# Kernel optimization log

Hardware: AMD Instinct MI355X
Metric: run time of the kernel (lower is better)

## Reference

```python
import jax, jax.numpy as jnp
import numpy as np

B, T, E = 4, 2048, 1024
H, D = 16, 64  # num_heads, head_size; H*D == E


def setup_inputs() -> dict:
    key = jax.random.key(0)
    ks = jax.random.split(key, 8)
    s = 0.02
    x = jax.random.normal(ks[0], (B, T, E), dtype=jnp.float32)
    attention_mask = jnp.ones((B, T), dtype=jnp.float32)
    # stacked per-head projection weights (no bias), torch Linear: y = x @ W.T
    Wq = jax.random.normal(ks[1], (H, E, D), dtype=jnp.float32) * s
    Wk = jax.random.normal(ks[2], (H, E, D), dtype=jnp.float32) * s
    Wv = jax.random.normal(ks[3], (H, E, D), dtype=jnp.float32) * s
    Wo = jax.random.normal(ks[4], (E, E), dtype=jnp.float32) * s
    bo = jnp.zeros((E,), dtype=jnp.float32)
    return {"x": x, "attention_mask": attention_mask, "Wq": Wq, "Wk": Wk,
            "Wv": Wv, "Wo": Wo, "bo": bo}


def reference(x, attention_mask, Wq, Wk, Wv, Wo, bo):
    # per-head projections, vectorized over heads: [B,T,E] x [H,E,D] -> [B,H,T,D]
    q = jnp.einsum('bte,hed->bhtd', x, Wq)
    k = jnp.einsum('bte,hed->bhtd', x, Wk)
    v = jnp.einsum('bte,hed->bhtd', x, Wv)
    scores = jnp.einsum('bhtd,bhsd->bhts', q, k) / jnp.sqrt(jnp.float32(D))
    # causal mask (tril): masked_fill with -inf
    causal = jnp.tril(jnp.ones((T, T), dtype=bool))
    scores = jnp.where(causal[None, None, :, :], scores, -jnp.inf)
    # padding mask: weights += (1 - mask) * finfo(float32).min, broadcast over queries
    neg = jnp.finfo(jnp.float32).min
    scores = scores + ((1.0 - attention_mask) * neg)[:, None, None, :]
    weights = jax.nn.softmax(scores, axis=-1)
    out = jnp.einsum('bhts,bhsd->bthd', weights, v).reshape(B, T, H * D)
    return out @ Wo.T + bo
```

## Files before the change

### kernel.cpp

```cpp
#include <hip/hip_runtime.h>
#include <hip/hip_bf16.h>

#define B_ 4
#define T_ 2048
#define E_ 1024
#define H_ 16
#define D_ 64
#define M_ (B_*T_)

typedef short bf16x8 __attribute__((ext_vector_type(8)));
typedef float f32x4  __attribute__((ext_vector_type(4)));
typedef float f32x16 __attribute__((ext_vector_type(16)));

__device__ __forceinline__ short f2bf(float f) {
    __hip_bfloat16 h = __float2bfloat16(f);
    return *reinterpret_cast<short*>(&h);
}

__device__ __forceinline__ void async_ld16(const void* g, void* l) {
    __builtin_amdgcn_global_load_lds(
        (const __attribute__((address_space(1))) unsigned int*)g,
        (__attribute__((address_space(3))) unsigned int*)l, 16, 0, 0);
}

__global__ void conv_bf16(const float* __restrict__ src, short* __restrict__ dst) {
    const int i = blockIdx.x * 256 + threadIdx.x;
    float4 v = ((const float4*)src)[i];
    short4 o = make_short4(f2bf(v.x), f2bf(v.y), f2bf(v.z), f2bf(v.w));
    ((short4*)dst)[i] = o;
}

__global__ void bias_prep(const float* __restrict__ mask, float* __restrict__ bias) {
    const int i = blockIdx.x * 256 + threadIdx.x;
    float bm = (1.0f - mask[i]) * -3.402823466e38f;
    bias[i] = fmaf(bm, 1.4426950f, -8.6561700f);
}

__global__ void wtrans(const float* __restrict__ Wq,
                       const float* __restrict__ Wk,
                       const float* __restrict__ Wv,
                       short* __restrict__ Wt) {
    const int which = blockIdx.z;
    const float* __restrict__ W = (which == 0) ? Wq : (which == 1) ? Wk : Wv;
    const int h  = blockIdx.y;
    const int e0 = blockIdx.x * 64;

    __shared__ float tile[64][65];
    const int tid = threadIdx.x;

#pragma unroll
    for (int r = 0; r < 4; ++r) {
        int lin = tid + r * 256;
        int er = lin >> 4, c4 = (lin & 15) * 4;
        float4 v = *(const float4*)(W + ((size_t)h * E_ + e0 + er) * D_ + c4);
        tile[er][c4 + 0] = v.x; tile[er][c4 + 1] = v.y;
        tile[er][c4 + 2] = v.z; tile[er][c4 + 3] = v.w;
    }
    __syncthreads();
#pragma unroll
    for (int r = 0; r < 4; ++r) {
        int lin = tid + r * 256;
        int dr = lin >> 4, j4 = (lin & 15) * 4;
        short4 o = make_short4(f2bf(tile[j4 + 0][dr]), f2bf(tile[j4 + 1][dr]),
                               f2bf(tile[j4 + 2][dr]), f2bf(tile[j4 + 3][dr]));
        *(short4*)(Wt + ((size_t)which * 1024 + h * 64 + dr) * E_ + e0 + j4) = o;
    }
}

template <int MODE>
__global__ __launch_bounds__(512, 2) void mfma_gemm(
        const short* __restrict__ A,
        const short* __restrict__ Bt,
        short* __restrict__ qo, short* __restrict__ ko, short* __restrict__ vo,
        float* __restrict__ Cout, const float* __restrict__ bo) {
    __shared__ __align__(16) char lds[3 * 49152];

    const int tid  = threadIdx.x;
    const int wave = tid >> 6, lane = tid & 63;
    const int c = lane & 15, quad = lane >> 4;
    const int wm = wave >> 1, wn = wave & 1;
    const int m0 = blockIdx.x * 256;
    const int n0 = blockIdx.y * 128;

    const int rr = tid >> 3;
    const int cc = (tid & 7) ^ (rr & 7);

    int aoff[4], boff[4];
#pragma unroll
    for (int mi = 0; mi < 4; ++mi) {
        int row = wm * 64 + mi * 16 + c;
        aoff[mi] = row * 128 + ((quad ^ (row & 7)) << 4);
    }
#pragma unroll
    for (int ni = 0; ni < 4; ++ni) {
        int row = wn * 64 + ni * 16 + c;
        boff[ni] = 32768 + row * 128 + ((quad ^ (row & 7)) << 4);
    }

    f32x4 acc[4][4] = {};

#define STGU(bufb, k0v, u) do {                                              \
        const short* _s = ((u) < 4) ? A : Bt;                                \
        const int _b0 = ((u) < 4) ? (m0 + (u) * 64) : (n0 + ((u) - 4) * 64); \
        const int _do = ((u) < 4) ? ((u) * 8192) : (32768 + ((u) - 4) * 8192);\
        async_ld16(_s + (size_t)(_b0 + rr) * 1024 + (k0v) + cc * 8,          \
                   lds + (bufb) + _do + wave * 1024);                        \
    } while (0)

#pragma unroll
    for (int u = 0; u < 6; ++u) STGU(0, 0, u);
#pragma unroll
    for (int u = 0; u < 6; ++u) STGU(49152, 64, u);
    asm volatile("s_waitcnt vmcnt(6)" ::: "memory");
    __builtin_amdgcn_s_barrier();

    int rbase = 0;
#pragma unroll 1
    for (int k = 0; k < 16; ++k) {
        const char* rb = lds + rbase;
        const int wbase = (rbase == 0) ? 98304 : rbase - 49152;
        const int kw = (k + 2) * 64;

        if (k < 14) {
            STGU(wbase, kw, 0); STGU(wbase, kw, 1);
            STGU(wbase, kw, 2); STGU(wbase, kw, 3);
            STGU(wbase, kw, 4); STGU(wbase, kw, 5);
        }

        bf16x8 a_[4][2], b_[4][2];
#pragma unroll
        for (int mi = 0; mi < 4; ++mi)
#pragma unroll
            for (int ks = 0; ks < 2; ++ks)
                a_[mi][ks] = *(const bf16x8*)(rb + (aoff[mi] ^ (ks << 6)));
#pragma unroll
        for (int ni = 0; ni < 4; ++ni)
#pragma unroll
            for (int ks = 0; ks < 2; ++ks)
                b_[ni][ks] = *(const bf16x8*)(rb + (boff[ni] ^ (ks << 6)));

        __builtin_amdgcn_s_setprio(1);
#pragma unroll
        for (int mi = 0; mi < 4; ++mi)
#pragma unroll
            for (int ni = 0; ni < 4; ++ni)
#pragma unroll
                for (int ks = 0; ks < 2; ++ks)
                    acc[mi][ni] = __builtin_amdgcn_mfma_f32_16x16x32_bf16(
                        a_[mi][ks], b_[ni][ks], acc[mi][ni], 0, 0, 0);
        __builtin_amdgcn_s_setprio(0);

        if (k < 14)       asm volatile("s_waitcnt vmcnt(6)" ::: "memory");
        else if (k == 14) asm volatile("s_waitcnt vmcnt(0)" ::: "memory");
        if (k < 15) __builtin_amdgcn_s_barrier();

        rbase = (rbase == 98304) ? 0 : rbase + 49152;
    }
#undef STGU

    if (MODE == 0) {
        const int which = n0 >> 10;
        const int nb = n0 & 1023;
        if (which == 2) {
#pragma unroll
            for (int mi = 0; mi < 4; ++mi) {
                const int m = m0 + wm * 64 + mi * 16 + quad * 4;
                const int b = m >> 11, t = m & 2047;
#pragma unroll
                for (int ni = 0; ni < 4; ++ni) {
                    const int n = nb + wn * 64 + ni * 16 + c;
                    const int h = n >> 6, d = n & 63;
                    short4 s4 = make_short4(f2bf(acc[mi][ni][0]), f2bf(acc[mi][ni][1]),
                                            f2bf(acc[mi][ni][2]), f2bf(acc[mi][ni][3]));
                    *(short4*)(vo + (((size_t)b * H_ + h) * D_ + d) * T_ + t) = s4;
                }
            }
        } else {
            short* __restrict__ outp = (which == 0) ? qo : ko;
            const float sc = (which == 0) ? 0.18033688f : 1.0f;
#pragma unroll
            for (int mi = 0; mi < 4; ++mi) {
#pragma unroll
                for (int i = 0; i < 4; ++i) {
                    const int m = m0 + wm * 64 + mi * 16 + quad * 4 + i;
                    const int b = m >> 11, t = m & 2047;
#pragma unroll
                    for (int ni = 0; ni < 4; ++ni) {
                        const int n = nb + wn * 64 + ni * 16 + c;
                        const int h = n >> 6, d = n & 63;
                        outp[(((size_t)b * H_ + h) * T_ + t) * D_ + d] =
                            f2bf(acc[mi][ni][i] * sc);
                    }
                }
            }
        }
    } else {
#pragma unroll
        for (int mi = 0; mi < 4; ++mi) {
#pragma unroll
            for (int i = 0; i < 4; ++i) {
                const int m = m0 + wm * 64 + mi * 16 + quad * 4 + i;
#pragma unroll
                for (int ni = 0; ni < 4; ++ni) {
                    const int n = n0 + wn * 64 + ni * 16 + c;
                    Cout[(size_t)m * E_ + n] = acc[mi][ni][i] + bo[n];
                }
            }
        }
    }
}

__global__ __launch_bounds__(256, 4) void flash_attn7(
        const short* __restrict__ qg,
        const short* __restrict__ kg,
        const short* __restrict__ vtg,
        const float* __restrict__ biasg,
        short* __restrict__ attn) {
    const int h = blockIdx.x, b = blockIdx.y;
    const int kb = 15 - blockIdx.z;
    const int tid  = threadIdx.x;
    const int wave = tid >> 6, lane = tid & 63;
    const int ln = lane & 31, hi = lane >> 5;
    const int q0w = kb * 128 + wave * 32;
    const int mytile = 4 * kb + wave;
    const int nt = 4 * kb + 4;

    __shared__ __align__(16) char lds[40960];

    const size_t bh = (size_t)b * H_ + h;
    const short* qbh  = qg  + bh * (size_t)T_ * D_;
    const short* kbh  = kg  + bh * (size_t)T_ * D_;
    const short* vtbh = vtg + bh * (size_t)D_ * T_;
    const float* biasb = biasg + (size_t)b * T_;

    const int ks = tid >> 3, kgs = (tid & 7) ^ (ks & 7);
    const int vd = tid >> 2, vgs = ((tid & 3) - (vd >> 1)) & 3;

    int kaddr[4];
#pragma unroll
    for (int kc = 0; kc < 4; ++kc)
        kaddr[kc] = ln * 128 + ((((kc << 1) + hi) ^ (ln & 7)) << 4);
    int vaddr[4];
#pragma unroll
    for (int dh = 0; dh < 2; ++dh)
#pragma unroll
        for (int kc2 = 0; kc2 < 2; ++kc2) {
            int d = dh * 32 + ln;
            vaddr[dh * 2 + kc2] =
                4096 + d * 64 + (((((kc2 << 1) + hi) + (d >> 1)) & 3) << 4);
        }

    bf16x8 qf[4];
#pragma unroll
    for (int kc = 0; kc < 4; ++kc)
        qf[kc] = *(const bf16x8*)(qbh + (size_t)(q0w + ln) * D_ + kc * 16 + hi * 8);

#pragma unroll
    for (int r = 0; r < 2; ++r)
        async_ld16(biasb + r * 1024 + tid * 4,
                   lds + 32768 + r * 4096 + wave * 1024);

#define STAGE_T(tt2) do {                                                   \
        const int _s0 = (tt2) << 5;                                         \
        const int _bb = ((tt2) & 3) * 8192;                                 \
        async_ld16(kbh + (size_t)(_s0 + ks) * D_ + (kgs << 3),              \
                   lds + _bb + wave * 1024);                                \
        async_ld16(vtbh + (size_t)vd * T_ + _s0 + (vgs << 3),               \
                   lds + _bb + 4096 + wave * 1024);                         \
    } while (0)

    STAGE_T(0);
    STAGE_T(1);

    f32x16 O0 = {}, O1 = {};
    float lacc = 0.0f;

    for (int tt = 0; tt < nt; ++tt) {
        if (tt + 2 < nt) STAGE_T(tt + 2);
        const int rem = nt - 1 - tt;
        if (rem >= 2)      asm volatile("s_waitcnt vmcnt(4)" ::: "memory");
        else if (rem == 1) asm volatile("s_waitcnt vmcnt(2)" ::: "memory");
        else               asm volatile("s_waitcnt vmcnt(0)" ::: "memory");
        __builtin_amdgcn_s_barrier();

        if (tt <= mytile) {
            const int s0 = tt << 5;
            const int bb = (tt & 3) * 8192;

            f32x4 b4[4];
#pragma unroll
            for (int g = 0; g < 4; ++g)
                b4[g] = *(const f32x4*)(lds + 32768 + (s0 + g * 8 + hi * 4) * 4);

            f32x16 S = {};
            __builtin_amdgcn_s_setprio(1);
#pragma unroll
            for (int kc = 0; kc < 4; ++kc) {
                bf16x8 ka = *(const bf16x8*)(lds + bb + kaddr[kc]);
                S = __builtin_amdgcn_mfma_f32_32x32x16_bf16(ka, qf[kc], S, 0, 0, 0);
            }
            __builtin_amdgcn_s_setprio(0);

            float p[16];
#pragma unroll
            for (int r = 0; r < 16; ++r) {
                float bb2 = ((const float*)&b4[r >> 2])[r & 3];
                p[r] = __builtin_amdgcn_exp2f(S[r] + bb2);
            }
            if (tt == mytile) {
#pragma unroll
                for (int r = 0; r < 16; ++r)
                    if (((r & 3) + ((r >> 2) << 3) + (hi << 2)) > ln)
                        p[r] = 0.0f;
            }
            {
                float t0 = (p[0] + p[1]) + (p[2] + p[3]);
                float t1 = (p[4] + p[5]) + (p[6] + p[7]);
                float t2s = (p[8] + p[9]) + (p[10] + p[11]);
                float t3 = (p[12] + p[13]) + (p[14] + p[15]);
                lacc += (t0 + t1) + (t2s + t3);
            }

            unsigned int u0, u1, u2, u3, u4, u5, u6, u7;
            asm("v_cvt_pk_bf16_f32 %0, %1, %2" : "=v"(u0) : "v"(p[0]),  "v"(p[1]));
            asm("v_cvt_pk_bf16_f32 %0, %1, %2" : "=v"(u1) : "v"(p[2]),  "v"(p[3]));
            asm("v_cvt_pk_bf16_f32 %0, %1, %2" : "=v"(u2) : "v"(p[4]),  "v"(p[5]));
            asm("v_cvt_pk_bf16_f32 %0, %1, %2" : "=v"(u3) : "v"(p[6]),  "v"(p[7]));
            asm("v_cvt_pk_bf16_f32 %0, %1, %2" : "=v"(u4) : "v"(p[8]),  "v"(p[9]));
            asm("v_cvt_pk_bf16_f32 %0, %1, %2" : "=v"(u5) : "v"(p[10]), "v"(p[11]));
            asm("v_cvt_pk_bf16_f32 %0, %1, %2" : "=v"(u6) : "v"(p[12]), "v"(p[13]));
            asm("v_cvt_pk_bf16_f32 %0, %1, %2" : "=v"(u7) : "v"(p[14]), "v"(p[15]));
            asm("v_permlane32_swap_b32 %0, %1" : "+v"(u0), "+v"(u2));
            asm("v_permlane32_swap_b32 %0, %1" : "+v"(u1), "+v"(u3));
            asm("v_permlane32_swap_b32 %0, %1" : "+v"(u4), "+v"(u6));
            asm("v_permlane32_swap_b32 %0, %1" : "+v"(u5), "+v"(u7));
            union { unsigned int w[4]; bf16x8 v; } pa0, pa1;
            pa0.w[0] = u0; pa0.w[1] = u1; pa0.w[2] = u2; pa0.w[3] = u3;
            pa1.w[0] = u4; pa1.w[1] = u5; pa1.w[2] = u6; pa1.w[3] = u7;

            bf16x8 v00 = *(const bf16x8*)(lds + bb + vaddr[0]);
            bf16x8 v01 = *(const bf16x8*)(lds + bb + vaddr[1]);
            bf16x8 v10 = *(const bf16x8*)(lds + bb + vaddr[2]);
            bf16x8 v11 = *(const bf16x8*)(lds + bb + vaddr[3]);
            __builtin_amdgcn_s_setprio(1);
            O0 = __builtin_amdgcn_mfma_f32_32x32x16_bf16(pa0.v, v00, O0, 0, 0, 0);
            O0 = __builtin_amdgcn_mfma_f32_32x32x16_bf16(pa1.v, v01, O0, 0, 0, 0);
            O1 = __builtin_amdgcn_mfma_f32_32x32x16_bf16(pa0.v, v10, O1, 0, 0, 0);
            O1 = __builtin_amdgcn_mfma_f32_32x32x16_bf16(pa1.v, v11, O1, 0, 0, 0);
            __builtin_amdgcn_s_setprio(0);
        }
    }
#undef STAGE_T

    unsigned int la = __float_as_uint(lacc), lb2 = la;
    asm("v_permlane32_swap_b32 %0, %1" : "+v"(la), "+v"(lb2));
    const float ltot = __uint_as_float(la) + __uint_as_float(lb2);

    __syncthreads();
    float* lsh = (float*)lds + wave * 32;
    if (hi == 0) lsh[ln] = 1.0f / ltot;
    __syncthreads();

    short* ab = attn + (size_t)b * T_ * E_ + h * D_;
#pragma unroll
    for (int r = 0; r < 16; ++r) {
        const int qrow = (r & 3) + ((r >> 2) << 3) + (hi << 2);
        const float iv = lsh[qrow];
        const size_t base = (size_t)(q0w + qrow) * E_;
        ab[base + ln]      = f2bf(O0[r] * iv);
        ab[base + 32 + ln] = f2bf(O1[r] * iv);
    }
}

extern "C" void kernel_launch(void* const* d_in, const int* in_sizes, int n_in,
                              void* d_out, int out_size, void* d_ws, size_t ws_size,
                              hipStream_t stream) {
    const float* x    = (const float*)d_in[0];
    const float* mask = (const float*)d_in[1];
    const float* Wq   = (const float*)d_in[2];
    const float* Wk   = (const float*)d_in[3];
    const float* Wv   = (const float*)d_in[4];
    const float* Wo   = (const float*)d_in[5];
    const float* bo   = (const float*)d_in[6];
    float* out        = (float*)d_out;

    const size_t S = (size_t)M_ * E_;
    char* ws = (char*)d_ws;
    short* xb   = (short*)ws;
    short* qb   = (short*)(ws + S * 2);
    short* kb   = (short*)(ws + S * 4);
    short* vtb  = (short*)(ws + S * 6);
    short* Wt   = (short*)(ws + S * 8);
    short* Wob  = (short*)(ws + S * 8 + (size_t)3 * 1024 * 1024 * 2);
    float* bias = (float*)(ws + S * 8 + (size_t)4 * 1024 * 1024 * 2);
    short* attnb = xb;

    conv_bf16<<<dim3(M_ * E_ / 1024), 256, 0, stream>>>(x, xb);
    conv_bf16<<<dim3(E_ * E_ / 1024), 256, 0, stream>>>(Wo, Wob);
    wtrans<<<dim3(E_ / 64, H_, 3), 256, 0, stream>>>(Wq, Wk, Wv, Wt);
    bias_prep<<<dim3(B_ * T_ / 256), 256, 0, stream>>>(mask, bias);

    mfma_gemm<0><<<dim3(M_ / 256, 3 * E_ / 128), 512, 0, stream>>>(
        xb, Wt, qb, kb, vtb, nullptr, nullptr);

    flash_attn7<<<dim3(H_, B_, 16), 256, 0, stream>>>(qb, kb, vtb, bias, attnb);

    mfma_gemm<1><<<dim3(M_ / 256, E_ / 128), 512, 0, stream>>>(
        attnb, Wob, nullptr, nullptr, nullptr, out, bo);
}
```

Baseline: 237.6 us.

## Fuse prep kernels into one launch and halve GEMM K-tile for higher occupancy

Merges the four preprocessing kernels (x/Wo bf16 conversion, QKV weight transpose, mask bias) into a single launch that dispatches on block index, removing three kernel launches and their gaps. The GEMM K-step drops from 64 to 32, which halves the triple-buffered LDS footprint and raises the launch-bounds occupancy hint from 2 to 4 blocks. The LDS swizzle and per-thread load mapping are redone for the narrower tile. In exchange the GEMM runs twice as many barriers and iterations with fewer MFMAs between each sync.

New measurement: 234.3 us. About the same (-1.4%).

```diff
diff --git a/kernel.cpp b/kernel.cpp
--- a/kernel.cpp
+++ b/kernel.cpp
@@ -23,57 +23,60 @@
         (__attribute__((address_space(3))) unsigned int*)l, 16, 0, 0);
 }
 
-__global__ void conv_bf16(const float* __restrict__ src, short* __restrict__ dst) {
-    const int i = blockIdx.x * 256 + threadIdx.x;
-    float4 v = ((const float4*)src)[i];
-    short4 o = make_short4(f2bf(v.x), f2bf(v.y), f2bf(v.z), f2bf(v.w));
-    ((short4*)dst)[i] = o;
-}
-
-__global__ void bias_prep(const float* __restrict__ mask, float* __restrict__ bias) {
-    const int i = blockIdx.x * 256 + threadIdx.x;
-    float bm = (1.0f - mask[i]) * -3.402823466e38f;
-    bias[i] = fmaf(bm, 1.4426950f, -8.6561700f);
-}
-
-__global__ void wtrans(const float* __restrict__ Wq,
-                       const float* __restrict__ Wk,
-                       const float* __restrict__ Wv,
-                       short* __restrict__ Wt) {
-    const int which = blockIdx.z;
-    const float* __restrict__ W = (which == 0) ? Wq : (which == 1) ? Wk : Wv;
-    const int h  = blockIdx.y;
-    const int e0 = blockIdx.x * 64;
-
+__global__ __launch_bounds__(256) void prep_fused(
+        const float* __restrict__ x,   const float* __restrict__ Wo,
+        const float* __restrict__ Wq,  const float* __restrict__ Wk,
+        const float* __restrict__ Wv,  const float* __restrict__ mask,
+        short* __restrict__ xb, short* __restrict__ Wob,
+        short* __restrict__ Wt, float* __restrict__ bias) {
     __shared__ float tile[64][65];
+    const int bi  = blockIdx.x;
     const int tid = threadIdx.x;
 
-#pragma unroll
-    for (int r = 0; r < 4; ++r) {
-        int lin = tid + r * 256;
-        int er = lin >> 4, c4 = (lin & 15) * 4;
-        float4 v = *(const float4*)(W + ((size_t)h * E_ + e0 + er) * D_ + c4);
-        tile[er][c4 + 0] = v.x; tile[er][c4 + 1] = v.y;
-        tile[er][c4 + 2] = v.z; tile[er][c4 + 3] = v.w;
-    }
-    __syncthreads();
-#pragma unroll
-    for (int r = 0; r < 4; ++r) {
-        int lin = tid + r * 256;
-        int dr = lin >> 4, j4 = (lin & 15) * 4;
-        short4 o = make_short4(f2bf(tile[j4 + 0][dr]), f2bf(tile[j4 + 1][dr]),
-                               f2bf(tile[j4 + 2][dr]), f2bf(tile[j4 + 3][dr]));
-        *(short4*)(Wt + ((size_t)which * 1024 + h * 64 + dr) * E_ + e0 + j4) = o;
+    if (bi < 9216) {
+        const float* src = (bi < 8192) ? x : Wo;
+        short* dst       = (bi < 8192) ? xb : Wob;
+        const int i = ((bi < 8192) ? bi : (bi - 8192)) * 256 + tid;
+        float4 v = ((const float4*)src)[i];
+        short4 o = make_short4(f2bf(v.x), f2bf(v.y), f2bf(v.z), f2bf(v.w));
+        ((short4*)dst)[i] = o;
+    } else if (bi < 9984) {
+        const int idx = bi - 9216;
+        const int which = idx >> 8;
+        const int h  = (idx & 255) >> 4;
+        const int e0 = (idx & 15) * 64;
+        const float* __restrict__ W = (which == 0) ? Wq : (which == 1) ? Wk : Wv;
+#pragma unroll
+        for (int r = 0; r < 4; ++r) {
+            int lin = tid + r * 256;
+            int er = lin >> 4, c4 = (lin & 15) * 4;
+            float4 v = *(const float4*)(W + ((size_t)h * E_ + e0 + er) * D_ + c4);
+            tile[er][c4 + 0] = v.x; tile[er][c4 + 1] = v.y;
+            tile[er][c4 + 2] = v.z; tile[er][c4 + 3] = v.w;
+        }
+        __syncthreads();
+#pragma unroll
+        for (int r = 0; r < 4; ++r) {
+            int lin = tid + r * 256;
+            int dr = lin >> 4, j4 = (lin & 15) * 4;
+            short4 o = make_short4(f2bf(tile[j4 + 0][dr]), f2bf(tile[j4 + 1][dr]),
+                                   f2bf(tile[j4 + 2][dr]), f2bf(tile[j4 + 3][dr]));
+            *(short4*)(Wt + ((size_t)which * 1024 + h * 64 + dr) * E_ + e0 + j4) = o;
+        }
+    } else {
+        const int i = (bi - 9984) * 256 + tid;
+        float bm = (1.0f - mask[i]) * -3.402823466e38f;
+        bias[i] = fmaf(bm, 1.4426950f, -8.6561700f);
     }
 }
 
 template <int MODE>
-__global__ __launch_bounds__(512, 2) void mfma_gemm(
+__global__ __launch_bounds__(512, 4) void mfma_gemm(
         const short* __restrict__ A,
         const short* __restrict__ Bt,
         short* __restrict__ qo, short* __restrict__ ko, short* __restrict__ vo,
         float* __restrict__ Cout, const float* __restrict__ bo) {
-    __shared__ __align__(16) char lds[3 * 49152];
+    __shared__ __align__(16) char lds[3 * 24576];
 
     const int tid  = threadIdx.x;
     const int wave = tid >> 6, lane = tid & 63;
@@ -82,81 +85,69 @@
     const int m0 = blockIdx.x * 256;
     const int n0 = blockIdx.y * 128;
 
-    const int rr = tid >> 3;
-    const int cc = (tid & 7) ^ (rr & 7);
+    const int ar = tid >> 2;
+    const int ag = (tid & 3) ^ ((tid >> 3) & 3);
 
     int aoff[4], boff[4];
 #pragma unroll
     for (int mi = 0; mi < 4; ++mi) {
         int row = wm * 64 + mi * 16 + c;
-        aoff[mi] = row * 128 + ((quad ^ (row & 7)) << 4);
+        aoff[mi] = row * 64 + ((quad ^ ((row >> 1) & 3)) << 4);
     }
 #pragma unroll
     for (int ni = 0; ni < 4; ++ni) {
         int row = wn * 64 + ni * 16 + c;
-        boff[ni] = 32768 + row * 128 + ((quad ^ (row & 7)) << 4);
+        boff[ni] = 16384 + row * 64 + ((quad ^ ((row >> 1) & 3)) << 4);
     }
 
     f32x4 acc[4][4] = {};
 
-#define STGU(bufb, k0v, u) do {                                              \
-        const short* _s = ((u) < 4) ? A : Bt;                                \
-        const int _b0 = ((u) < 4) ? (m0 + (u) * 64) : (n0 + ((u) - 4) * 64); \
-        const int _do = ((u) < 4) ? ((u) * 8192) : (32768 + ((u) - 4) * 8192);\
-        async_ld16(_s + (size_t)(_b0 + rr) * 1024 + (k0v) + cc * 8,          \
-                   lds + (bufb) + _do + wave * 1024);                        \
+#define STG(bufb, k0v) do {                                                  \
+        async_ld16(A  + (size_t)(m0 + ar) * 1024 + (k0v) + ag * 8,           \
+                   lds + (bufb) + wave * 1024);                              \
+        async_ld16(A  + (size_t)(m0 + 128 + ar) * 1024 + (k0v) + ag * 8,     \
+                   lds + (bufb) + 8192 + wave * 1024);                       \
+        async_ld16(Bt + (size_t)(n0 + ar) * 1024 + (k0v) + ag * 8,           \
+                   lds + (bufb) + 16384 + wave * 1024);                      \
     } while (0)
 
-#pragma unroll
-    for (int u = 0; u < 6; ++u) STGU(0, 0, u);
-#pragma unroll
-    for (int u = 0; u < 6; ++u) STGU(49152, 64, u);
-    asm volatile("s_waitcnt vmcnt(6)" ::: "memory");
+    STG(0, 0);
+    STG(24576, 32);
+    asm volatile("s_waitcnt vmcnt(3)" ::: "memory");
     __builtin_amdgcn_s_barrier();
 
     int rbase = 0;
 #pragma unroll 1
-    for (int k = 0; k < 16; ++k) {
+    for (int k = 0; k < 32; ++k) {
         const char* rb = lds + rbase;
-        const int wbase = (rbase == 0) ? 98304 : rbase - 49152;
-        const int kw = (k + 2) * 64;
-
-        if (k < 14) {
-            STGU(wbase, kw, 0); STGU(wbase, kw, 1);
-            STGU(wbase, kw, 2); STGU(wbase, kw, 3);
-            STGU(wbase, kw, 4); STGU(wbase, kw, 5);
-        }
-
-        bf16x8 a_[4][2], b_[4][2];
+        const int wbase = (rbase == 0) ? 49152 : rbase - 24576;
+
+        if (k < 30) STG(wbase, (k + 2) * 32);
+
+        bf16x8 a_[4], b_[4];
 #pragma unroll
         for (int mi = 0; mi < 4; ++mi)
-#pragma unroll
-            for (int ks = 0; ks < 2; ++ks)
-                a_[mi][ks] = *(const bf16x8*)(rb + (aoff[mi] ^ (ks << 6)));
+            a_[mi] = *(const bf16x8*)(rb + aoff[mi]);
 #pragma unroll
         for (int ni = 0; ni < 4; ++ni)
-#pragma unroll
-            for (int ks = 0; ks < 2; ++ks)
-                b_[ni][ks] = *(const bf16x8*)(rb + (boff[ni] ^ (ks << 6)));
+            b_[ni] = *(const bf16x8*)(rb + boff[ni]);
 
         __builtin_amdgcn_s_setprio(1);
 #pragma unroll
         for (int mi = 0; mi < 4; ++mi)
 #pragma unroll
             for (int ni = 0; ni < 4; ++ni)
-#pragma unroll
-                for (int ks = 0; ks < 2; ++ks)
-                    acc[mi][ni] = __builtin_amdgcn_mfma_f32_16x16x32_bf16(
-                        a_[mi][ks], b_[ni][ks], acc[mi][ni], 0, 0, 0);
+                acc[mi][ni] = __builtin_amdgcn_mfma_f32_16x16x32_bf16(
+                    a_[mi], b_[ni], acc[mi][ni], 0, 0, 0);
         __builtin_amdgcn_s_setprio(0);
 
-        if (k < 14)       asm volatile("s_waitcnt vmcnt(6)" ::: "memory");
-        else if (k == 14) asm volatile("s_waitcnt vmcnt(0)" ::: "memory");
-        if (k < 15) __builtin_amdgcn_s_barrier();
-
-        rbase = (rbase == 98304) ? 0 : rbase + 49152;
-    }
-#undef STGU
+        if (k < 30)       asm volatile("s_waitcnt vmcnt(3)" ::: "memory");
+        else if (k == 30) asm volatile("s_waitcnt vmcnt(0)" ::: "memory");
+        if (k < 31) __builtin_amdgcn_s_barrier();
+
+        rbase = (rbase == 49152) ? 0 : rbase + 24576;
+    }
+#undef STG
 
     if (MODE == 0) {
         const int which = n0 >> 10;
@@ -395,10 +386,8 @@
     float* bias = (float*)(ws + S * 8 + (size_t)4 * 1024 * 1024 * 2);
     short* attnb = xb;
 
-    conv_bf16<<<dim3(M_ * E_ / 1024), 256, 0, stream>>>(x, xb);
-    conv_bf16<<<dim3(E_ * E_ / 1024), 256, 0, stream>>>(Wo, Wob);
-    wtrans<<<dim3(E_ / 64, H_, 3), 256, 0, stream>>>(Wq, Wk, Wv, Wt);
-    bias_prep<<<dim3(B_ * T_ / 256), 256, 0, stream>>>(mask, bias);
+    prep_fused<<<dim3(10016), 256, 0, stream>>>(
+        x, Wo, Wq, Wk, Wv, mask, xb, Wob, Wt, bias);
 
     mfma_gemm<0><<<dim3(M_ / 256, 3 * E_ / 128), 512, 0, stream>>>(
         xb, Wt, qb, kb, vtb, nullptr, nullptr);
```
